# Kernel optimization log

Measured on AMD Instinct MI355X. Metric: run time of the kernel, lower is better.

Reference implementation:

```python
import jax, jax.numpy as jnp
import numpy as np

N = 50000      # nodes
E = 500000     # edges (avg in-degree 10)
DIN = 256      # in_dim
D = 128        # out_dim


def setup_inputs() -> dict:
    key = jax.random.key(0)
    ks = jax.random.split(key, 8)
    x = jax.random.normal(ks[0], (N, DIN), jnp.float32)
    efeat = jax.random.normal(ks[1], (E, D), jnp.float32)
    att_node = jax.random.uniform(ks[2], (N,), jnp.float32)
    att_edge = jax.random.uniform(ks[3], (E,), jnp.float32)
    src = jax.random.randint(ks[4], (E,), 0, N, dtype=jnp.int32)
    # every node gets in-degree >= 1 (DGL skips zero-in-degree nodes in reduce)
    dst = (jnp.arange(E, dtype=jnp.int32) % N)
    Wn = jax.random.normal(ks[5], (D, DIN), jnp.float32) * (1.0 / np.sqrt(DIN))
    bn = jnp.zeros((D,), jnp.float32)
    Wa = jax.random.normal(ks[6], (D, 3 * D), jnp.float32) * (1.0 / np.sqrt(3 * D))
    ba = jnp.zeros((D,), jnp.float32)
    return {"x": x, "efeat": efeat, "att_node": att_node, "att_edge": att_edge,
            "src": src, "dst": dst, "Wn": Wn, "bn": bn, "Wa": Wa, "ba": ba}


def reference(x, efeat, att_node, att_edge, src, dst, Wn, bn, Wa, ba):
    # apply_node: node feat = node_fc(feat)                      [N, D]
    h = x @ Wn.T + bn
    # message: z1 = att_src * src_feat, z2 = att_e * edge_feat   [E, 2D]
    z1 = att_node[src][:, None] * h[src]
    z2 = att_edge[:, None] * efeat
    msg = jnp.concatenate([z1, z2], axis=1)
    # reduce: scatter-sum messages to dst nodes                  [N, 2D]
    agg = jax.ops.segment_sum(msg, dst, num_segments=N)
    # relu(apply_fc_node(cat[msg_sum, h])) scaled by node att    [N, D]
    r = jax.nn.relu(jnp.concatenate([agg, h], axis=1) @ Wa.T + ba)
    return att_node[:, None] * r
```

## Files before the change

kernel.cpp:

```cpp
#include <hip/hip_runtime.h>
#include <hip/hip_bf16.h>

#define NN 50000
#define EE 500000
#define KEDGE 10

typedef unsigned short u16;
typedef unsigned int u32;
using f32x4  = __attribute__((ext_vector_type(4))) float;
using bf16x8 = __attribute__((ext_vector_type(8))) short;

#define OF_WFT   0
#define OF_BF    32768
#define OF_WABT  33024
#define OF_G     41216

__device__ __forceinline__ u16 f2bfc(float f) {
    return __bfloat16_as_ushort(__float2bfloat16(f));
}
__device__ __forceinline__ u32 pk2(float a, float b) {
    return (u32)f2bfc(a) | ((u32)f2bfc(b) << 16);
}
__device__ __forceinline__ float bflo(u32 g) { return __uint_as_float(g << 16); }
__device__ __forceinline__ float bfhi(u32 g) { return __uint_as_float(g & 0xffff0000u); }

__global__ void k_fuse_w(const float* __restrict__ Wn, const float* __restrict__ bn,
                         const float* __restrict__ Wa, u16* __restrict__ WfT,
                         float* __restrict__ bf, u16* __restrict__ WaBfT) {
    int jp = blockIdx.x;
    if (jp < 256) {
        int jj  = jp & 127;
        int off = (jp < 128) ? 0 : 256;
        int k = threadIdx.x;
        float a0 = 0.f, a1 = 0.f, a2 = 0.f, a3 = 0.f;
        for (int i = 0; i < 128; i += 4) {
            a0 = fmaf(Wn[(i + 0) * 256 + k], Wa[jj * 384 + off + i + 0], a0);
            a1 = fmaf(Wn[(i + 1) * 256 + k], Wa[jj * 384 + off + i + 1], a1);
            a2 = fmaf(Wn[(i + 2) * 256 + k], Wa[jj * 384 + off + i + 2], a2);
            a3 = fmaf(Wn[(i + 3) * 256 + k], Wa[jj * 384 + off + i + 3], a3);
        }
        WfT[jp * 256 + k] = f2bfc((a0 + a1) + (a2 + a3));
    } else if (jp == 256) {
        int j = threadIdx.x;
        int jj  = j & 127;
        int off = (j < 128) ? 0 : 256;
        float acc = 0.f;
        for (int i = 0; i < 128; ++i)
            acc = fmaf(bn[i], Wa[jj * 384 + off + i], acc);
        bf[j] = acc;
    } else {
        for (int i = threadIdx.x; i < 16384; i += 256) {
            int j = i >> 7, k = i & 127;
            WaBfT[i] = f2bfc(Wa[j * 384 + 128 + k]);
        }
    }
}

__global__ __launch_bounds__(512) void k_gemm_G(const float* __restrict__ x,
                                                const u16* __restrict__ WfT,
                                                const float* __restrict__ bf,
                                                u16* __restrict__ G) {
    __shared__ __align__(16) u16 As[128 * 64];
    __shared__ __align__(16) u16 Bs[256 * 64];
    const int t  = threadIdx.x;
    const int m0 = blockIdx.x * 128;
    const int w  = t >> 6, l = t & 63;
    const int wm = w >> 2, wn = w & 3;
    const int lr = l & 15, lg = l >> 4;
    f32x4 acc[4][4];
#pragma unroll
    for (int a = 0; a < 4; ++a)
#pragma unroll
        for (int b = 0; b < 4; ++b) { acc[a][b][0]=0.f; acc[a][b][1]=0.f; acc[a][b][2]=0.f; acc[a][b][3]=0.f; }

    for (int kt = 0; kt < 256; kt += 64) {
#pragma unroll
        for (int p = 0; p < 4; ++p) {
            int f   = t + p * 512;
            int row = f >> 4, c4 = f & 15;
            int gm  = m0 + row;
            float4 v = make_float4(0.f, 0.f, 0.f, 0.f);
            if (gm < NN) v = *(const float4*)(x + (long)gm * 256 + kt + c4 * 4);
            int byte = (row * 128 + c4 * 8) ^ ((row & 7) << 4);
            *(uint2*)((char*)As + byte) = make_uint2(pk2(v.x, v.y), pk2(v.z, v.w));
        }
#pragma unroll
        for (int p = 0; p < 4; ++p) {
            int f   = t + p * 512;
            int row = f >> 3, sl = f & 7;
            uint4 v = *(const uint4*)(WfT + (long)row * 256 + kt + sl * 8);
            int byte = (row * 128 + sl * 16) ^ ((row & 7) << 4);
            *(uint4*)((char*)Bs + byte) = v;
        }
        __syncthreads();
#pragma unroll
        for (int kk = 0; kk < 2; ++kk) {
            bf16x8 av[4], bv[4];
#pragma unroll
            for (int a = 0; a < 4; ++a) {
                int row = wm * 64 + a * 16 + lr;
                int byte = (row * 128 + kk * 64 + lg * 16) ^ ((row & 7) << 4);
                av[a] = *(bf16x8*)((char*)As + byte);
            }
#pragma unroll
            for (int b = 0; b < 4; ++b) {
                int row = wn * 64 + b * 16 + lr;
                int byte = (row * 128 + kk * 64 + lg * 16) ^ ((row & 7) << 4);
                bv[b] = *(bf16x8*)((char*)Bs + byte);
            }
#pragma unroll
            for (int a = 0; a < 4; ++a)
#pragma unroll
                for (int b = 0; b < 4; ++b)
                    acc[a][b] = __builtin_amdgcn_mfma_f32_16x16x32_bf16(av[a], bv[b], acc[a][b], 0, 0, 0);
        }
        __syncthreads();
    }
#pragma unroll
    for (int b = 0; b < 4; ++b) {
        int n = wn * 64 + b * 16 + lr;
        float bias = bf[n];
#pragma unroll
        for (int a = 0; a < 4; ++a) {
            int mbase = m0 + wm * 64 + a * 16 + lg * 4;
#pragma unroll
            for (int r = 0; r < 4; ++r) {
                int m = mbase + r;
                if (m < NN) G[(long)m * 256 + n] = f2bfc(acc[a][b][r] + bias);
            }
        }
    }
}

__global__ __launch_bounds__(512) void k_fused_out(const u16* __restrict__ G,
                                                   const float* __restrict__ efeat,
                                                   const float* __restrict__ att_node,
                                                   const float* __restrict__ att_edge,
                                                   const int* __restrict__ src,
                                                   const u16* __restrict__ WaBfT,
                                                   const float* __restrict__ ba,
                                                   float* __restrict__ out) {
    __shared__ __align__(16) char smem[80896];
    char*  AsB = smem;
    char*  BsB = smem + 32768;
    char*  PB  = smem;
    int*   sS  = (int*)(smem + 65536);
    float* sA  = (float*)(smem + 70656);
    float* sE  = (float*)(smem + 75776);

    const int t  = threadIdx.x;
    const int n0 = blockIdx.x * 128;
    const int w  = t >> 6, l = t & 63;
    const int wm = w >> 2, wn = w & 3;
    const int lr = l & 15, lg = l >> 4;

    for (int i = t; i < 1280; i += 512) {
        int k = i >> 7, m = i & 127;
        int n = n0 + m;
        int s = 0; float a = 0.f, ev = 0.f;
        if (n < NN) {
            int e = n + k * NN;
            s  = src[e];
            a  = att_node[s];
            ev = att_edge[e];
        }
        sS[i] = s; sA[i] = a; sE[i] = ev;
    }
#pragma unroll
    for (int p = 0; p < 4; ++p) {
        int f   = t + p * 512;
        int row = f >> 4, sl = f & 15;
        uint4 v = *(const uint4*)(WaBfT + row * 128 + sl * 8);
        int byte = (row * 256 + sl * 16) ^ ((row & 7) << 4);
        *(uint4*)(BsB + byte) = v;
    }
    __syncthreads();

    {
        const int jq = t & 31;
        const int mr = t >> 5;
#pragma unroll 1
        for (int p = 0; p < 8; ++p) {
            int m = mr + p * 16;
            int n = n0 + m;
            float4 acc4 = make_float4(0.f, 0.f, 0.f, 0.f);
            if (n < NN) {
#pragma unroll
                for (int k = 0; k < KEDGE; ++k) {
                    float aE = sE[k * 128 + m];
                    float4 v = *(const float4*)(efeat + (long)(n + k * NN) * 128 + jq * 4);
                    acc4.x = fmaf(aE, v.x, acc4.x);
                    acc4.y = fmaf(aE, v.y, acc4.y);
                    acc4.z = fmaf(aE, v.z, acc4.z);
                    acc4.w = fmaf(aE, v.w, acc4.w);
                }
            }
            int byte = (m * 256 + jq * 8) ^ ((m & 7) << 4);
            *(uint2*)(AsB + byte) = make_uint2(pk2(acc4.x, acc4.y), pk2(acc4.z, acc4.w));
        }
    }
    __syncthreads();

    f32x4 acc[4][2];
#pragma unroll
    for (int a = 0; a < 4; ++a)
#pragma unroll
        for (int b = 0; b < 2; ++b) { acc[a][b][0]=0.f; acc[a][b][1]=0.f; acc[a][b][2]=0.f; acc[a][b][3]=0.f; }
#pragma unroll
    for (int kk = 0; kk < 4; ++kk) {
        bf16x8 av[4], bv[2];
#pragma unroll
        for (int a = 0; a < 4; ++a) {
            int row = wm * 64 + a * 16 + lr;
            int byte = (row * 256 + kk * 64 + lg * 16) ^ ((row & 7) << 4);
            av[a] = *(bf16x8*)(AsB + byte);
        }
#pragma unroll
        for (int b = 0; b < 2; ++b) {
            int row = wn * 32 + b * 16 + lr;
            int byte = (row * 256 + kk * 64 + lg * 16) ^ ((row & 7) << 4);
            bv[b] = *(bf16x8*)(BsB + byte);
        }
#pragma unroll
        for (int a = 0; a < 4; ++a)
#pragma unroll
            for (int b = 0; b < 2; ++b)
                acc[a][b] = __builtin_amdgcn_mfma_f32_16x16x32_bf16(av[a], bv[b], acc[a][b], 0, 0, 0);
    }
    __syncthreads();

    {
        const int jq = t & 31;
        const int mr = t >> 5;
#pragma unroll 1
        for (int p = 0; p < 8; ++p) {
            int m = mr + p * 16;
            int n = n0 + m;
            float4 acc4 = make_float4(0.f, 0.f, 0.f, 0.f);
            if (n < NN) {
                uint2 g3 = *(const uint2*)(G + (long)n * 256 + 128 + jq * 4);
                acc4.x = bflo(g3.x); acc4.y = bfhi(g3.x);
                acc4.z = bflo(g3.y); acc4.w = bfhi(g3.y);
#pragma unroll
                for (int k = 0; k < KEDGE; ++k) {
                    float aS = sA[k * 128 + m];
                    uint2 g  = *(const uint2*)(G + (long)sS[k * 128 + m] * 256 + jq * 4);
                    acc4.x = fmaf(aS, bflo(g.x), acc4.x);
                    acc4.y = fmaf(aS, bfhi(g.x), acc4.y);
                    acc4.z = fmaf(aS, bflo(g.y), acc4.z);
                    acc4.w = fmaf(aS, bfhi(g.y), acc4.w);
                }
            }
            int byte = (m * 512 + jq * 16) ^ ((m & 7) << 4);
            *(float4*)(PB + byte) = acc4;
        }
    }
    __syncthreads();

#pragma unroll
    for (int a = 0; a < 4; ++a) {
#pragma unroll
        for (int r = 0; r < 4; ++r) {
            int m  = wm * 64 + a * 16 + lg * 4 + r;
            int gm = n0 + m;
            if (gm < NN) {
                float attn = att_node[gm];
#pragma unroll
                for (int b = 0; b < 2; ++b) {
                    int n = wn * 32 + b * 16 + lr;
                    float pv = *(const float*)(PB + ((m * 512 + n * 4) ^ ((m & 7) << 4)));
                    float val = acc[a][b][r] + pv + ba[n];
                    out[(long)gm * 128 + n] = attn * fmaxf(val, 0.f);
                }
            }
        }
    }
}

extern "C" void kernel_launch(void* const* d_in, const int* in_sizes, int n_in,
                              void* d_out, int out_size, void* d_ws, size_t ws_size,
                              hipStream_t stream) {
    const float* x        = (const float*)d_in[0];
    const float* efeat    = (const float*)d_in[1];
    const float* att_node = (const float*)d_in[2];
    const float* att_edge = (const float*)d_in[3];
    const int*   src      = (const int*)d_in[4];
    const float* Wn       = (const float*)d_in[6];
    const float* bn       = (const float*)d_in[7];
    const float* Wa       = (const float*)d_in[8];
    const float* ba       = (const float*)d_in[9];
    float* out = (float*)d_out;

    float* ws    = (float*)d_ws;
    u16*   WfT   = (u16*)(ws + OF_WFT);
    float* bf    = ws + OF_BF;
    u16*   WaBfT = (u16*)(ws + OF_WABT);
    u16*   G     = (u16*)(ws + OF_G);

    hipLaunchKernelGGL(k_fuse_w, dim3(258), dim3(256), 0, stream, Wn, bn, Wa, WfT, bf, WaBfT);
    hipLaunchKernelGGL(k_gemm_G, dim3(391), dim3(512), 0, stream, x, WfT, bf, G);
    hipLaunchKernelGGL(k_fused_out, dim3(391), dim3(512), 0, stream, G, efeat, att_node,
                       att_edge, src, WaBfT, ba, out);
}
```

Before: 137.8 us.

## Split edge-feature aggregation into a streaming kernel and shrink GEMM tiles

Moves the efeat weighted reduction out of the fused output kernel into a separate grid-stride streaming kernel. That kernel writes a bf16 aggregate and packs src index with att_node[src] into a meta array. The GEMM and output kernels switch to 64-row tiles with 256 threads, doubling the block count for better occupancy and load balance, and k_fuse_w is restructured to use shared memory and a split-K reduction. The cost is an extra kernel launch plus a round trip through global memory for the bf16 aggregate and the meta array.

```diff
diff --git a/kernel.cpp b/kernel.cpp
--- a/kernel.cpp
+++ b/kernel.cpp
@@ -14,6 +14,8 @@
 #define OF_BF    32768
 #define OF_WABT  33024
 #define OF_G     41216
+#define OF_AGG2  (OF_G + NN * 128)
+#define OF_META  (OF_AGG2 + NN * 64)
 
 __device__ __forceinline__ u16 f2bfc(float f) {
     return __bfloat16_as_ushort(__float2bfloat16(f));
@@ -24,48 +26,95 @@
 __device__ __forceinline__ float bflo(u32 g) { return __uint_as_float(g << 16); }
 __device__ __forceinline__ float bfhi(u32 g) { return __uint_as_float(g & 0xffff0000u); }
 
-__global__ void k_fuse_w(const float* __restrict__ Wn, const float* __restrict__ bn,
-                         const float* __restrict__ Wa, u16* __restrict__ WfT,
-                         float* __restrict__ bf, u16* __restrict__ WaBfT) {
+__global__ __launch_bounds__(512) void k_fuse_w(const float* __restrict__ Wn,
+                                                const float* __restrict__ bn,
+                                                const float* __restrict__ Wa,
+                                                u16* __restrict__ WfT,
+                                                float* __restrict__ bf,
+                                                u16* __restrict__ WaBfT) {
     int jp = blockIdx.x;
     if (jp < 256) {
+        __shared__ float wrow[128];
+        __shared__ float red[256];
         int jj  = jp & 127;
         int off = (jp < 128) ? 0 : 256;
-        int k = threadIdx.x;
-        float a0 = 0.f, a1 = 0.f, a2 = 0.f, a3 = 0.f;
-        for (int i = 0; i < 128; i += 4) {
-            a0 = fmaf(Wn[(i + 0) * 256 + k], Wa[jj * 384 + off + i + 0], a0);
-            a1 = fmaf(Wn[(i + 1) * 256 + k], Wa[jj * 384 + off + i + 1], a1);
-            a2 = fmaf(Wn[(i + 2) * 256 + k], Wa[jj * 384 + off + i + 2], a2);
-            a3 = fmaf(Wn[(i + 3) * 256 + k], Wa[jj * 384 + off + i + 3], a3);
-        }
-        WfT[jp * 256 + k] = f2bfc((a0 + a1) + (a2 + a3));
-    } else if (jp == 256) {
-        int j = threadIdx.x;
-        int jj  = j & 127;
-        int off = (j < 128) ? 0 : 256;
-        float acc = 0.f;
-        for (int i = 0; i < 128; ++i)
-            acc = fmaf(bn[i], Wa[jj * 384 + off + i], acc);
-        bf[j] = acc;
+        int tt  = threadIdx.x;
+        if (tt < 128) wrow[tt] = Wa[jj * 384 + off + tt];
+        __syncthreads();
+        int k  = tt & 255, ih = tt >> 8;
+        int i0 = ih * 64;
+        float a0 = 0.f, a1 = 0.f;
+        for (int i = i0; i < i0 + 64; i += 2) {
+            a0 = fmaf(Wn[(i + 0) * 256 + k], wrow[i + 0], a0);
+            a1 = fmaf(Wn[(i + 1) * 256 + k], wrow[i + 1], a1);
+        }
+        float s = a0 + a1;
+        if (ih) red[k] = s;
+        __syncthreads();
+        if (!ih) WfT[jp * 256 + k] = f2bfc(s + red[k]);
     } else {
-        for (int i = threadIdx.x; i < 16384; i += 256) {
-            int j = i >> 7, k = i & 127;
-            WaBfT[i] = f2bfc(Wa[j * 384 + 128 + k]);
-        }
-    }
-}
-
-__global__ __launch_bounds__(512) void k_gemm_G(const float* __restrict__ x,
+        int tt = threadIdx.x;
+        if (tt < 256) {
+            int j   = tt;
+            int jj  = j & 127;
+            int off = (j < 128) ? 0 : 256;
+            float acc = 0.f;
+            for (int i = 0; i < 128; ++i)
+                acc = fmaf(bn[i], Wa[jj * 384 + off + i], acc);
+            bf[j] = acc;
+        } else {
+            for (int i = tt - 256; i < 16384; i += 256) {
+                int j = i >> 7, k = i & 127;
+                WaBfT[i] = f2bfc(Wa[j * 384 + 128 + k]);
+            }
+        }
+    }
+}
+
+#define NAGG  2048
+#define NMETA 128
+__global__ __launch_bounds__(256) void k_edge_stream(const float* __restrict__ efeat,
+                                                     const float* __restrict__ att_edge,
+                                                     const int* __restrict__ src,
+                                                     const float* __restrict__ att_node,
+                                                     u16* __restrict__ agg2,
+                                                     uint2* __restrict__ meta) {
+    int bid = blockIdx.x;
+    if (bid < NAGG) {
+        for (int q = bid * 256 + threadIdx.x; q < NN * 32; q += NAGG * 256) {
+            int n  = q >> 5;
+            int j4 = q & 31;
+            float4 a = make_float4(0.f, 0.f, 0.f, 0.f);
+#pragma unroll
+            for (int k = 0; k < KEDGE; ++k) {
+                int e = n + k * NN;
+                float aE = att_edge[e];
+                float4 v = *(const float4*)(efeat + (long)e * 128 + j4 * 4);
+                a.x = fmaf(aE, v.x, a.x);
+                a.y = fmaf(aE, v.y, a.y);
+                a.z = fmaf(aE, v.z, a.z);
+                a.w = fmaf(aE, v.w, a.w);
+            }
+            *(uint2*)(agg2 + (long)n * 128 + j4 * 4) =
+                make_uint2(pk2(a.x, a.y), pk2(a.z, a.w));
+        }
+    } else {
+        for (int e = (bid - NAGG) * 256 + threadIdx.x; e < EE; e += NMETA * 256) {
+            int s = src[e];
+            meta[e] = make_uint2((u32)s, __float_as_uint(att_node[s]));
+        }
+    }
+}
+
+__global__ __launch_bounds__(256) void k_gemm_G(const float* __restrict__ x,
                                                 const u16* __restrict__ WfT,
                                                 const float* __restrict__ bf,
                                                 u16* __restrict__ G) {
-    __shared__ __align__(16) u16 As[128 * 64];
+    __shared__ __align__(16) u16 As[64 * 64];
     __shared__ __align__(16) u16 Bs[256 * 64];
     const int t  = threadIdx.x;
-    const int m0 = blockIdx.x * 128;
-    const int w  = t >> 6, l = t & 63;
-    const int wm = w >> 2, wn = w & 3;
+    const int m0 = blockIdx.x * 64;
+    const int wn = t >> 6, l = t & 63;
     const int lr = l & 15, lg = l >> 4;
     f32x4 acc[4][4];
 #pragma unroll
@@ -76,7 +125,7 @@
     for (int kt = 0; kt < 256; kt += 64) {
 #pragma unroll
         for (int p = 0; p < 4; ++p) {
-            int f   = t + p * 512;
+            int f   = t + p * 256;
             int row = f >> 4, c4 = f & 15;
             int gm  = m0 + row;
             float4 v = make_float4(0.f, 0.f, 0.f, 0.f);
@@ -85,8 +134,8 @@
             *(uint2*)((char*)As + byte) = make_uint2(pk2(v.x, v.y), pk2(v.z, v.w));
         }
 #pragma unroll
-        for (int p = 0; p < 4; ++p) {
-            int f   = t + p * 512;
+        for (int p = 0; p < 8; ++p) {
+            int f   = t + p * 256;
             int row = f >> 3, sl = f & 7;
             uint4 v = *(const uint4*)(WfT + (long)row * 256 + kt + sl * 8);
             int byte = (row * 128 + sl * 16) ^ ((row & 7) << 4);
@@ -98,7 +147,7 @@
             bf16x8 av[4], bv[4];
 #pragma unroll
             for (int a = 0; a < 4; ++a) {
-                int row = wm * 64 + a * 16 + lr;
+                int row = a * 16 + lr;
                 int byte = (row * 128 + kk * 64 + lg * 16) ^ ((row & 7) << 4);
                 av[a] = *(bf16x8*)((char*)As + byte);
             }
@@ -122,7 +171,7 @@
         float bias = bf[n];
 #pragma unroll
         for (int a = 0; a < 4; ++a) {
-            int mbase = m0 + wm * 64 + a * 16 + lg * 4;
+            int mbase = m0 + a * 16 + lg * 4;
 #pragma unroll
             for (int r = 0; r < 4; ++r) {
                 int m = mbase + r;
@@ -132,47 +181,66 @@
     }
 }
 
-__global__ __launch_bounds__(512) void k_fused_out(const u16* __restrict__ G,
-                                                   const float* __restrict__ efeat,
-                                                   const float* __restrict__ att_node,
-                                                   const float* __restrict__ att_edge,
-                                                   const int* __restrict__ src,
-                                                   const u16* __restrict__ WaBfT,
-                                                   const float* __restrict__ ba,
-                                                   float* __restrict__ out) {
-    __shared__ __align__(16) char smem[80896];
-    char*  AsB = smem;
-    char*  BsB = smem + 32768;
-    char*  PB  = smem;
-    int*   sS  = (int*)(smem + 65536);
-    float* sA  = (float*)(smem + 70656);
-    float* sE  = (float*)(smem + 75776);
-
+__global__ __launch_bounds__(256) void k_gemm_out(const u16* __restrict__ G,
+                                                  const u16* __restrict__ agg2,
+                                                  const uint2* __restrict__ meta,
+                                                  const u16* __restrict__ WaBfT,
+                                                  const float* __restrict__ att_node,
+                                                  const float* __restrict__ ba,
+                                                  float* __restrict__ out) {
+    __shared__ __align__(16) u16 As[64 * 128];
+    __shared__ __align__(16) u16 Bs[128 * 128];
+    char* PB = (char*)Bs;
     const int t  = threadIdx.x;
-    const int n0 = blockIdx.x * 128;
-    const int w  = t >> 6, l = t & 63;
-    const int wm = w >> 2, wn = w & 3;
+    const int n0 = blockIdx.x * 64;
+    const int wn = t >> 6, l = t & 63;
     const int lr = l & 15, lg = l >> 4;
 
-    for (int i = t; i < 1280; i += 512) {
-        int k = i >> 7, m = i & 127;
-        int n = n0 + m;
-        int s = 0; float a = 0.f, ev = 0.f;
-        if (n < NN) {
-            int e = n + k * NN;
-            s  = src[e];
-            a  = att_node[s];
-            ev = att_edge[e];
-        }
-        sS[i] = s; sA[i] = a; sE[i] = ev;
-    }
 #pragma unroll
     for (int p = 0; p < 4; ++p) {
-        int f   = t + p * 512;
+        int f   = t + p * 256;
+        int row = f >> 4, sl = f & 15;
+        int gm  = n0 + row;
+        uint4 v = make_uint4(0u, 0u, 0u, 0u);
+        if (gm < NN) v = *(const uint4*)(agg2 + (long)gm * 128 + sl * 8);
+        int byte = (row * 256 + sl * 16) ^ ((row & 7) << 4);
+        *(uint4*)((char*)As + byte) = v;
+    }
+#pragma unroll
+    for (int p = 0; p < 8; ++p) {
+        int f   = t + p * 256;
         int row = f >> 4, sl = f & 15;
         uint4 v = *(const uint4*)(WaBfT + row * 128 + sl * 8);
         int byte = (row * 256 + sl * 16) ^ ((row & 7) << 4);
-        *(uint4*)(BsB + byte) = v;
+        *(uint4*)((char*)Bs + byte) = v;
+    }
+    __syncthreads();
+
+    f32x4 acc[4][2];
+#pragma unroll
+    for (int a = 0; a < 4; ++a)
+#pragma unroll
+        for (int b = 0; b < 2; ++b) { acc[a][b][0]=0.f; acc[a][b][1]=0.f; acc[a][b][2]=0.f; acc[a][b][3]=0.f; }
+#pragma unroll
+    for (int kk = 0; kk < 4; ++kk) {
+        bf16x8 av[4], bv[2];
+#pragma unroll
+        for (int a = 0; a < 4; ++a) {
+            int row = a * 16 + lr;
+            int byte = (row * 256 + kk * 64 + lg * 16) ^ ((row & 7) << 4);
+            av[a] = *(bf16x8*)((char*)As + byte);
+        }
+#pragma unroll
+        for (int b = 0; b < 2; ++b) {
+            int row = wn * 32 + b * 16 + lr;
+            int byte = (row * 256 + kk * 64 + lg * 16) ^ ((row & 7) << 4);
+            bv[b] = *(bf16x8*)((char*)Bs + byte);
+        }
+#pragma unroll
+        for (int a = 0; a < 4; ++a)
+#pragma unroll
+            for (int b = 0; b < 2; ++b)
+                acc[a][b] = __builtin_amdgcn_mfma_f32_16x16x32_bf16(av[a], bv[b], acc[a][b], 0, 0, 0);
     }
     __syncthreads();
 
@@ -181,78 +249,26 @@
         const int mr = t >> 5;
 #pragma unroll 1
         for (int p = 0; p < 8; ++p) {
-            int m = mr + p * 16;
+            int m = mr + p * 8;
             int n = n0 + m;
-            float4 acc4 = make_float4(0.f, 0.f, 0.f, 0.f);
-            if (n < NN) {
-#pragma unroll
-                for (int k = 0; k < KEDGE; ++k) {
-                    float aE = sE[k * 128 + m];
-                    float4 v = *(const float4*)(efeat + (long)(n + k * NN) * 128 + jq * 4);
-                    acc4.x = fmaf(aE, v.x, acc4.x);
-                    acc4.y = fmaf(aE, v.y, acc4.y);
-                    acc4.z = fmaf(aE, v.z, acc4.z);
-                    acc4.w = fmaf(aE, v.w, acc4.w);
-                }
-            }
-            int byte = (m * 256 + jq * 8) ^ ((m & 7) << 4);
-            *(uint2*)(AsB + byte) = make_uint2(pk2(acc4.x, acc4.y), pk2(acc4.z, acc4.w));
-        }
-    }
-    __syncthreads();
-
-    f32x4 acc[4][2];
-#pragma unroll
-    for (int a = 0; a < 4; ++a)
-#pragma unroll
-        for (int b = 0; b < 2; ++b) { acc[a][b][0]=0.f; acc[a][b][1]=0.f; acc[a][b][2]=0.f; acc[a][b][3]=0.f; }
-#pragma unroll
-    for (int kk = 0; kk < 4; ++kk) {
-        bf16x8 av[4], bv[2];
-#pragma unroll
-        for (int a = 0; a < 4; ++a) {
-            int row = wm * 64 + a * 16 + lr;
-            int byte = (row * 256 + kk * 64 + lg * 16) ^ ((row & 7) << 4);
-            av[a] = *(bf16x8*)(AsB + byte);
-        }
-#pragma unroll
-        for (int b = 0; b < 2; ++b) {
-            int row = wn * 32 + b * 16 + lr;
-            int byte = (row * 256 + kk * 64 + lg * 16) ^ ((row & 7) << 4);
-            bv[b] = *(bf16x8*)(BsB + byte);
-        }
-#pragma unroll
-        for (int a = 0; a < 4; ++a)
-#pragma unroll
-            for (int b = 0; b < 2; ++b)
-                acc[a][b] = __builtin_amdgcn_mfma_f32_16x16x32_bf16(av[a], bv[b], acc[a][b], 0, 0, 0);
-    }
-    __syncthreads();
-
-    {
-        const int jq = t & 31;
-        const int mr = t >> 5;
-#pragma unroll 1
-        for (int p = 0; p < 8; ++p) {
-            int m = mr + p * 16;
-            int n = n0 + m;
-            float4 acc4 = make_float4(0.f, 0.f, 0.f, 0.f);
+            float4 a4 = make_float4(0.f, 0.f, 0.f, 0.f);
             if (n < NN) {
                 uint2 g3 = *(const uint2*)(G + (long)n * 256 + 128 + jq * 4);
-                acc4.x = bflo(g3.x); acc4.y = bfhi(g3.x);
-                acc4.z = bflo(g3.y); acc4.w = bfhi(g3.y);
+                a4.x = bflo(g3.x); a4.y = bfhi(g3.x);
+                a4.z = bflo(g3.y); a4.w = bfhi(g3.y);
 #pragma unroll
                 for (int k = 0; k < KEDGE; ++k) {
-                    float aS = sA[k * 128 + m];
-                    uint2 g  = *(const uint2*)(G + (long)sS[k * 128 + m] * 256 + jq * 4);
-                    acc4.x = fmaf(aS, bflo(g.x), acc4.x);
-                    acc4.y = fmaf(aS, bfhi(g.x), acc4.y);
-                    acc4.z = fmaf(aS, bflo(g.y), acc4.z);
-                    acc4.w = fmaf(aS, bfhi(g.y), acc4.w);
+                    uint2 me = meta[n + k * NN];
+                    float aS = __uint_as_float(me.y);
+                    uint2 g  = *(const uint2*)(G + (long)me.x * 256 + jq * 4);
+                    a4.x = fmaf(aS, bflo(g.x), a4.x);
+                    a4.y = fmaf(aS, bfhi(g.x), a4.y);
+                    a4.z = fmaf(aS, bflo(g.y), a4.z);
+                    a4.w = fmaf(aS, bfhi(g.y), a4.w);
                 }
             }
             int byte = (m * 512 + jq * 16) ^ ((m & 7) << 4);
-            *(float4*)(PB + byte) = acc4;
+            *(float4*)(PB + byte) = a4;
         }
     }
     __syncthreads();
@@ -261,7 +277,7 @@
     for (int a = 0; a < 4; ++a) {
 #pragma unroll
         for (int r = 0; r < 4; ++r) {
-            int m  = wm * 64 + a * 16 + lg * 4 + r;
+            int m  = a * 16 + lg * 4 + r;
             int gm = n0 + m;
             if (gm < NN) {
                 float attn = att_node[gm];
@@ -296,9 +312,13 @@
     float* bf    = ws + OF_BF;
     u16*   WaBfT = (u16*)(ws + OF_WABT);
     u16*   G     = (u16*)(ws + OF_G);
-
-    hipLaunchKernelGGL(k_fuse_w, dim3(258), dim3(256), 0, stream, Wn, bn, Wa, WfT, bf, WaBfT);
-    hipLaunchKernelGGL(k_gemm_G, dim3(391), dim3(512), 0, stream, x, WfT, bf, G);
-    hipLaunchKernelGGL(k_fused_out, dim3(391), dim3(512), 0, stream, G, efeat, att_node,
-                       att_edge, src, WaBfT, ba, out);
-}
+    u16*   agg2  = (u16*)(ws + OF_AGG2);
+    uint2* meta  = (uint2*)(ws + OF_META);
+
+    hipLaunchKernelGGL(k_fuse_w, dim3(257), dim3(512), 0, stream, Wn, bn, Wa, WfT, bf, WaBfT);
+    hipLaunchKernelGGL(k_edge_stream, dim3(NAGG + NMETA), dim3(256), 0, stream,
+                       efeat, att_edge, src, att_node, agg2, meta);
+    hipLaunchKernelGGL(k_gemm_G, dim3(782), dim3(256), 0, stream, x, WfT, bf, G);
+    hipLaunchKernelGGL(k_gemm_out, dim3(782), dim3(256), 0, stream, G, agg2, meta, WaBfT,
+                       att_node, ba, out);
+}
```

Measured after the change: 167.4 us. 1.21x slower.
